# Kernel tuning notes

Hardware: AMD Instinct MI355X
Metric: run time of the kernel (lower is better)

## Reference

```python
import jax, jax.numpy as jnp
import numpy as np

B, S, D, H, L, I, V, T = 8, 512, 768, 12, 6, 3072, 30522, 2
DH = D // H  # 64


def ln2d(x, g, b, eps=1e-5):
    # LayerNorm over the last two dims ([S, D]), affine params shaped [S, D]
    mu = jnp.mean(x, axis=(-2, -1), keepdims=True)
    var = jnp.var(x, axis=(-2, -1), keepdims=True)
    return (x - mu) * jax.lax.rsqrt(var + eps) * g + b


def setup_inputs() -> dict:
    key = jax.random.key(0)
    ks = jax.random.split(key, 16)
    s = 0.02
    inp = {
        "input_ids": jax.random.randint(ks[0], (B, S), 0, V, dtype=jnp.int32),
        "segment_ids": jax.random.randint(ks[1], (B, S), 0, T, dtype=jnp.int32),
        "input_mask": jnp.ones((B, S), dtype=jnp.float32),
        "word_emb": jax.random.normal(ks[2], (V, D), jnp.float32) * s,
        "seg_emb": jax.random.normal(ks[3], (T, D), jnp.float32) * s,
        "pos_emb": jax.random.normal(ks[4], (S, D), jnp.float32) * s,
        "ln0_g": jnp.ones((S, D), jnp.float32),
        "ln0_b": jnp.zeros((S, D), jnp.float32),
        "Wq": jax.random.normal(ks[5], (L, D, D), jnp.float32) * s,
        "Wk": jax.random.normal(ks[6], (L, D, D), jnp.float32) * s,
        "Wv": jax.random.normal(ks[7], (L, D, D), jnp.float32) * s,
        "W1": jax.random.normal(ks[8], (L, D, D), jnp.float32) * s,
        "b1": jnp.zeros((L, D), jnp.float32),
        "Wi": jax.random.normal(ks[9], (L, D, I), jnp.float32) * s,
        "bi": jnp.zeros((L, I), jnp.float32),
        "W2": jax.random.normal(ks[10], (L, I, D), jnp.float32) * s,
        "b2": jnp.zeros((L, D), jnp.float32),
        "lng": jnp.ones((L, S, D), jnp.float32),
        "lnb": jnp.zeros((L, S, D), jnp.float32),
        "Wp": jax.random.normal(ks[11], (D, 2), jnp.float32) * s,
        "bp": jnp.zeros((2,), jnp.float32),
    }
    return inp


def _forward(input_ids, segment_ids, input_mask, word_emb, seg_emb, pos_emb,
             ln0_g, ln0_b, Wq, Wk, Wv, W1, b1, Wi, bi, W2, b2, lng, lnb, Wp, bp):
    # embedding (word + segment + position), then 2-D LayerNorm
    x = word_emb[input_ids] + seg_emb[segment_ids] + pos_emb  # [B,S,D]
    x = ln2d(x, ln0_g, ln0_b)
    # multiplicative attention mask, broadcast over heads and KEY axis
    qmask = input_mask[:, None, :, None]  # [B,1,S,1]
    scale = 1.0 / jnp.sqrt(jnp.asarray(DH, x.dtype))
    for l in range(L):
        prev = x
        q = (x @ Wq[l]).reshape(B, S, H, DH).transpose(0, 2, 1, 3)
        k = (x @ Wk[l]).reshape(B, S, H, DH).transpose(0, 2, 1, 3)
        v = (x @ Wv[l]).reshape(B, S, H, DH).transpose(0, 2, 1, 3)
        scores = jnp.einsum('bhqd,bhkd->bhqk', q, k) * scale
        scores = scores * qmask  # multiplicative mask (as in source)
        probs = jax.nn.softmax(scores, axis=-1)
        attn = jnp.einsum('bhqk,bhkd->bhqd', probs, v)
        attn = attn.transpose(0, 2, 1, 3).reshape(B, S, D)
        h = jax.nn.relu(attn @ W1[l] + b1[l])
        h = jax.nn.relu(h @ Wi[l] + bi[l])
        h = jax.nn.relu(h @ W2[l] + b2[l])
        x = ln2d(h + prev, lng[l], lnb[l])
    logits = x @ Wp + bp  # [B,S,2]
    logits = logits + (1.0 - input_mask)[:, :, None] * (-1e4)
    return logits[:, :, 0], logits[:, :, 1]


def reference(input_ids, segment_ids, input_mask, word_emb, seg_emb, pos_emb,
              ln0_g, ln0_b, Wq, Wk, Wv, W1, b1, Wi, bi, W2, b2, lng, lnb, Wp, bp):
    return _forward(input_ids, segment_ids, input_mask, word_emb, seg_emb, pos_emb,
                    ln0_g, ln0_b, Wq, Wk, Wv, W1, b1, Wi, bi, W2, b2, lng, lnb, Wp, bp)
```

## Files before the change

### kernel.cpp

```cpp
#include <hip/hip_runtime.h>
#include <cstdint>
#include <cstddef>

typedef __bf16 bf16x8 __attribute__((ext_vector_type(8)));
typedef float f32x4 __attribute__((ext_vector_type(4)));
typedef unsigned short u16;

#define NB 8
#define NS 512
#define ND 768
#define NH 12
#define NL 6
#define NI 3072
#define NROWS (NB*NS)
#define SD (NS*ND)
#define MN ((size_t)NROWS*ND)

__device__ __forceinline__ u16 f2bf(float f) {
  union { float f; unsigned u; } v; v.f = f;
  unsigned r = v.u + 0x7fffu + ((v.u >> 16) & 1u);
  return (u16)(r >> 16);
}

#define GLL(gsrc, ldst) \
  __builtin_amdgcn_global_load_lds((__attribute__((address_space(1))) void*)(gsrc), \
                                   (__attribute__((address_space(3))) void*)(ldst), 16, 0, 0)

__global__ __launch_bounds__(256) void wconv_k(
    const float* __restrict__ Wq, const float* __restrict__ Wk, const float* __restrict__ Wv,
    const float* __restrict__ W1, const float* __restrict__ Wi, const float* __restrict__ W2,
    u16* __restrict__ wqkv_t, u16* __restrict__ w1_t, u16* __restrict__ wi_t, u16* __restrict__ w2_t)
{
  int bid = blockIdx.x;
  int l = bid / 1728, r = bid % 1728;
  const float* src; u16* dst; int Csrc, dstLD, tr, tc;
  if (r < 432) {
    int which = r / 144, t = r % 144;
    src = (which == 0 ? Wq : (which == 1 ? Wk : Wv)) + (size_t)l * ND * ND;
    dst = wqkv_t + (size_t)l * 2304 * ND + (size_t)which * ND * ND;
    Csrc = ND; dstLD = ND; tr = t / 12; tc = t % 12;
  } else if (r < 576) {
    int t = r - 432;
    src = W1 + (size_t)l * ND * ND; dst = w1_t + (size_t)l * ND * ND;
    Csrc = ND; dstLD = ND; tr = t / 12; tc = t % 12;
  } else if (r < 1152) {
    int t = r - 576;
    src = Wi + (size_t)l * ND * NI; dst = wi_t + (size_t)l * ND * NI;
    Csrc = NI; dstLD = ND; tr = t / 48; tc = t % 48;
  } else {
    int t = r - 1152;
    src = W2 + (size_t)l * ND * NI; dst = w2_t + (size_t)l * ND * NI;
    Csrc = ND; dstLD = NI; tr = t / 12; tc = t % 12;
  }
  __shared__ u16 tile[64][65];
  int t0 = threadIdx.x;
  int rr = t0 >> 2, c4 = (t0 & 3) * 16;
  const float* sp = src + (size_t)(tr * 64 + rr) * Csrc + tc * 64 + c4;
  #pragma unroll
  for (int q = 0; q < 4; q++) {
    float4 v = reinterpret_cast<const float4*>(sp)[q];
    tile[rr][c4 + q * 4 + 0] = f2bf(v.x);
    tile[rr][c4 + q * 4 + 1] = f2bf(v.y);
    tile[rr][c4 + q * 4 + 2] = f2bf(v.z);
    tile[rr][c4 + q * 4 + 3] = f2bf(v.w);
  }
  __syncthreads();
  int cc = t0 >> 2, r4 = (t0 & 3) * 16;
  u16* dp = dst + (size_t)(tc * 64 + cc) * dstLD + tr * 64 + r4;
  unsigned res[8];
  #pragma unroll
  for (int e = 0; e < 8; e++)
    res[e] = (unsigned)tile[r4 + 2 * e][cc] | ((unsigned)tile[r4 + 2 * e + 1][cc] << 16);
  reinterpret_cast<uint4*>(dp)[0] = make_uint4(res[0], res[1], res[2], res[3]);
  reinterpret_cast<uint4*>(dp + 8)[0] = make_uint4(res[4], res[5], res[6], res[7]);
}

__global__ void embed_k(const int* __restrict__ ids, const int* __restrict__ segs,
    const float* __restrict__ wemb, const float* __restrict__ semb, const float* __restrict__ pemb,
    float* __restrict__ out)
{
  int row = blockIdx.x;
  int s = row & (NS - 1);
  int t = threadIdx.x;
  int id = ids[row], sg = segs[row];
  float4 a = reinterpret_cast<const float4*>(wemb + (size_t)id * ND)[t];
  float4 b = reinterpret_cast<const float4*>(semb + (size_t)sg * ND)[t];
  float4 c = reinterpret_cast<const float4*>(pemb + (size_t)s * ND)[t];
  float4 o;
  o.x = a.x + b.x + c.x; o.y = a.y + b.y + c.y; o.z = a.z + b.z + c.z; o.w = a.w + b.w + c.w;
  reinterpret_cast<float4*>(out + (size_t)row * ND)[t] = o;
}

__global__ __launch_bounds__(256) void ln_part_k(const float* __restrict__ x, float* __restrict__ part)
{
  int b = blockIdx.x >> 6, c = blockIdx.x & 63;
  const float* base = x + (size_t)b * SD + c * 6144;
  int t = threadIdx.x;
  float s = 0.f, sq = 0.f;
  #pragma unroll
  for (int j = 0; j < 6; j++) {
    float4 v = reinterpret_cast<const float4*>(base)[t + j * 256];
    s += v.x + v.y + v.z + v.w;
    sq += v.x * v.x + v.y * v.y + v.z * v.z + v.w * v.w;
  }
  #pragma unroll
  for (int d = 1; d < 64; d <<= 1) { s += __shfl_xor(s, d); sq += __shfl_xor(sq, d); }
  __shared__ float red[8];
  int w = t >> 6, lane = t & 63;
  if (lane == 0) { red[w] = s; red[4 + w] = sq; }
  __syncthreads();
  if (t == 0) {
    part[blockIdx.x * 2 + 0] = red[0] + red[1] + red[2] + red[3];
    part[blockIdx.x * 2 + 1] = red[4] + red[5] + red[6] + red[7];
  }
}

__global__ void ln_final_k(const float* __restrict__ part, float* __restrict__ mv)
{
  int b = blockIdx.x;
  int lane = threadIdx.x;
  float s = part[(b * 64 + lane) * 2 + 0];
  float q = part[(b * 64 + lane) * 2 + 1];
  #pragma unroll
  for (int d = 1; d < 64; d <<= 1) { s += __shfl_xor(s, d); q += __shfl_xor(q, d); }
  if (lane == 0) {
    float inv = 1.f / (float)SD;
    float mu = s * inv;
    float var = q * inv - mu * mu;
    mv[b * 2 + 0] = mu;
    mv[b * 2 + 1] = rsqrtf(var + 1e-5f);
  }
}

__global__ __launch_bounds__(256) void ln_apply_k(const float* __restrict__ x,
    const float* __restrict__ g, const float* __restrict__ bta, const float* __restrict__ mv,
    float* __restrict__ xf, u16* __restrict__ xb)
{
  int idx = blockIdx.x * 256 + threadIdx.x;
  int e = idx * 4;
  int b = e / SD;
  int sd = e - b * SD;
  float mu = mv[b * 2 + 0], rstd = mv[b * 2 + 1];
  float4 v = reinterpret_cast<const float4*>(x)[idx];
  float4 gg = reinterpret_cast<const float4*>(g)[sd >> 2];
  float4 bb = reinterpret_cast<const float4*>(bta)[sd >> 2];
  float y0 = (v.x - mu) * rstd * gg.x + bb.x;
  float y1 = (v.y - mu) * rstd * gg.y + bb.y;
  float y2 = (v.z - mu) * rstd * gg.z + bb.z;
  float y3 = (v.w - mu) * rstd * gg.w + bb.w;
  float4 o; o.x = y0; o.y = y1; o.z = y2; o.w = y3;
  reinterpret_cast<float4*>(xf)[idx] = o;
  reinterpret_cast<ushort4*>(xb)[idx] = make_ushort4(f2bf(y0), f2bf(y1), f2bf(y2), f2bf(y3));
}

__global__ __launch_bounds__(256) void finw2_k(const float* __restrict__ P,
    const float* __restrict__ bias, const float* __restrict__ resid,
    float* __restrict__ ln_in, float* __restrict__ part)
{
  int b = blockIdx.x >> 6, c = blockIdx.x & 63;
  size_t f4base = ((size_t)b * SD + (size_t)c * 6144) >> 2;
  int t = threadIdx.x;
  float s = 0.f, sq = 0.f;
  #pragma unroll
  for (int j = 0; j < 6; j++) {
    size_t fi = f4base + t + j * 256;
    float4 p0 = reinterpret_cast<const float4*>(P)[fi];
    float4 p1 = reinterpret_cast<const float4*>(P)[fi + (MN >> 2)];
    float4 p2 = reinterpret_cast<const float4*>(P)[fi + 2 * (MN >> 2)];
    float4 p3 = reinterpret_cast<const float4*>(P)[fi + 3 * (MN >> 2)];
    float4 rv = reinterpret_cast<const float4*>(resid)[fi];
    int col4 = (((t + j * 256) * 4) % ND) >> 2;
    float4 bv = reinterpret_cast<const float4*>(bias)[col4];
    float y0 = fmaxf(p0.x + p1.x + p2.x + p3.x + bv.x, 0.f) + rv.x;
    float y1 = fmaxf(p0.y + p1.y + p2.y + p3.y + bv.y, 0.f) + rv.y;
    float y2 = fmaxf(p0.z + p1.z + p2.z + p3.z + bv.z, 0.f) + rv.z;
    float y3 = fmaxf(p0.w + p1.w + p2.w + p3.w + bv.w, 0.f) + rv.w;
    float4 o; o.x = y0; o.y = y1; o.z = y2; o.w = y3;
    reinterpret_cast<float4*>(ln_in)[fi] = o;
    s += y0 + y1 + y2 + y3;
    sq += y0 * y0 + y1 * y1 + y2 * y2 + y3 * y3;
  }
  #pragma unroll
  for (int d = 1; d < 64; d <<= 1) { s += __shfl_xor(s, d); sq += __shfl_xor(sq, d); }
  __shared__ float red[8];
  int w = t >> 6, lane = t & 63;
  if (lane == 0) { red[w] = s; red[4 + w] = sq; }
  __syncthreads();
  if (t == 0) {
    part[blockIdx.x * 2 + 0] = red[0] + red[1] + red[2] + red[3];
    part[blockIdx.x * 2 + 1] = red[4] + red[5] + red[6] + red[7];
  }
}

#define BM 128
#define BN 128
#define BK 32

template<int EPI>
__global__ __launch_bounds__(256) void gemm_bt(
    const u16* __restrict__ A, const u16* __restrict__ Bt, void* __restrict__ Cv,
    const float* __restrict__ bias, int M, int N, int K)
{
  __shared__ __align__(16) u16 As[BM * BK];
  __shared__ __align__(16) u16 Bs[BN * BK];
  const int t = threadIdx.x;
  const int lane = t & 63, w = t >> 6;
  const int wr = w >> 1, wc = w & 1;
  const int l15 = lane & 15, lh = lane >> 4;
  const int m0 = blockIdx.y * BM, n0 = blockIdx.x * BN;
  const int Ksub = K / gridDim.z;
  const int Koff = blockIdx.z * Ksub;

  f32x4 acc[4][4];
  const f32x4 z4 = {0.f, 0.f, 0.f, 0.f};
  #pragma unroll
  for (int i = 0; i < 4; i++)
    #pragma unroll
    for (int j = 0; j < 4; j++) acc[i][j] = z4;

  const int ca = t, cb = t + 256;
  const u16* a0p = A + (size_t)(m0 + (ca >> 2)) * K + (ca & 3) * 8;
  const u16* a1p = A + (size_t)(m0 + (cb >> 2)) * K + (cb & 3) * 8;
  const u16* b0p = Bt + (size_t)(n0 + (ca >> 2)) * K + (ca & 3) * 8;
  const u16* b1p = Bt + (size_t)(n0 + (cb >> 2)) * K + (cb & 3) * 8;
  u16* la0 = As + ca * 8; u16* la1 = As + cb * 8;
  u16* lb0 = Bs + ca * 8; u16* lb1 = Bs + cb * 8;

  for (int k0 = Koff; k0 < Koff + Ksub; k0 += BK) {
    __syncthreads();
    GLL(a0p + k0, la0);
    GLL(a1p + k0, la1);
    GLL(b0p + k0, lb0);
    GLL(b1p + k0, lb1);
    __syncthreads();
    bf16x8 af[4], bfr[4];
    #pragma unroll
    for (int i = 0; i < 4; i++)
      af[i] = *reinterpret_cast<const bf16x8*>(&As[(wr * 64 + i * 16 + l15) * BK + lh * 8]);
    #pragma unroll
    for (int j = 0; j < 4; j++)
      bfr[j] = *reinterpret_cast<const bf16x8*>(&Bs[(wc * 64 + j * 16 + l15) * BK + lh * 8]);
    #pragma unroll
    for (int i = 0; i < 4; i++)
      #pragma unroll
      for (int j = 0; j < 4; j++)
        acc[i][j] = __builtin_amdgcn_mfma_f32_16x16x32_bf16(af[i], bfr[j], acc[i][j], 0, 0, 0);
  }

  float* Pout = (float*)Cv + (size_t)blockIdx.z * M * N;
  #pragma unroll
  for (int i = 0; i < 4; i++) {
    int row_b = m0 + wr * 64 + i * 16 + lh * 4;
    #pragma unroll
    for (int j = 0; j < 4; j++) {
      int col = n0 + wc * 64 + j * 16 + l15;
      float bv = (EPI == 1) ? bias[col] : 0.f;
      #pragma unroll
      for (int r = 0; r < 4; r++) {
        size_t off = (size_t)(row_b + r) * N + col;
        float v = acc[i][j][r];
        if (EPI == 1) ((u16*)Cv)[off] = f2bf(fmaxf(v + bv, 0.f));
        else if (EPI == 3) Pout[off] = v;
        else ((u16*)Cv)[off] = f2bf(v);
      }
    }
  }
}

__global__ __launch_bounds__(256) void attn_k(
    const u16* __restrict__ qkv, const float* __restrict__ mask, u16* __restrict__ out)
{
  const int qt = blockIdx.x;
  const int h = blockIdx.y;
  const int b = blockIdx.z;
  __shared__ __align__(16) u16 Qs[128 * 64];
  __shared__ __align__(16) u16 Ks[64 * 72];
  __shared__ __align__(16) u16 Vt[64 * 72];
  __shared__ __align__(16) u16 Pw[4][32 * 72];
  const int t = threadIdx.x, lane = t & 63, w = t >> 6;
  const int l15 = lane & 15, lh = lane >> 4;

  #pragma unroll
  for (int p = 0; p < 4; p++) {
    int c = t + p * 256;
    const u16* src = qkv + (size_t)(b * NS + qt * 128 + (c >> 3)) * 2304 + h * 64 + (c & 7) * 8;
    GLL(src, Qs + c * 8);
  }
  __syncthreads();

  bf16x8 aq[2][2];
  #pragma unroll
  for (int i = 0; i < 2; i++)
    #pragma unroll
    for (int kk = 0; kk < 2; kk++)
      aq[i][kk] = *reinterpret_cast<const bf16x8*>(&Qs[(w * 32 + i * 16 + l15) * 64 + kk * 32 + lh * 8]);

  float qm[2][4];
  #pragma unroll
  for (int i = 0; i < 2; i++)
    #pragma unroll
    for (int r = 0; r < 4; r++)
      qm[i][r] = mask[b * NS + qt * 128 + w * 32 + i * 16 + lh * 4 + r] * 0.125f;

  float mrun[2][4], lrun[2][4];
  f32x4 o[2][4];
  const f32x4 z4 = {0.f, 0.f, 0.f, 0.f};
  #pragma unroll
  for (int i = 0; i < 2; i++)
    #pragma unroll
    for (int r = 0; r < 4; r++) { mrun[i][r] = -3e38f; lrun[i][r] = 0.f; }
  #pragma unroll
  for (int i = 0; i < 2; i++)
    #pragma unroll
    for (int jn = 0; jn < 4; jn++) o[i][jn] = z4;

  for (int kc = 0; kc < 8; kc++) {
    __syncthreads();
    #pragma unroll
    for (int p = 0; p < 2; p++) {
      int k = (t >> 3) + p * 32;
      int dh0 = (t & 7) * 8;
      const u16* ks = qkv + (size_t)(b * NS + kc * 64 + k) * 2304 + ND + h * 64 + dh0;
      uint4 kv4 = *reinterpret_cast<const uint4*>(ks);
      *reinterpret_cast<uint4*>(&Ks[k * 72 + dh0]) = kv4;
    }
    #pragma unroll
    for (int p = 0; p < 2; p++) {
      int k = (t >> 3) + p * 32;
      int dh0 = (t & 7) * 8;
      const u16* vs = qkv + (size_t)(b * NS + kc * 64 + k) * 2304 + 2 * ND + h * 64 + dh0;
      uint4 vv = *reinterpret_cast<const uint4*>(vs);
      Vt[(dh0 + 0) * 72 + k] = (u16)(vv.x & 0xffff);
      Vt[(dh0 + 1) * 72 + k] = (u16)(vv.x >> 16);
      Vt[(dh0 + 2) * 72 + k] = (u16)(vv.y & 0xffff);
      Vt[(dh0 + 3) * 72 + k] = (u16)(vv.y >> 16);
      Vt[(dh0 + 4) * 72 + k] = (u16)(vv.z & 0xffff);
      Vt[(dh0 + 5) * 72 + k] = (u16)(vv.z >> 16);
      Vt[(dh0 + 6) * 72 + k] = (u16)(vv.w & 0xffff);
      Vt[(dh0 + 7) * 72 + k] = (u16)(vv.w >> 16);
    }
    __syncthreads();

    f32x4 s[2][4];
    #pragma unroll
    for (int i = 0; i < 2; i++)
      #pragma unroll
      for (int j = 0; j < 4; j++) s[i][j] = z4;
    #pragma unroll
    for (int kk = 0; kk < 2; kk++) {
      bf16x8 bk[4];
      #pragma unroll
      for (int j = 0; j < 4; j++)
        bk[j] = *reinterpret_cast<const bf16x8*>(&Ks[(j * 16 + l15) * 72 + kk * 32 + lh * 8]);
      #pragma unroll
      for (int i = 0; i < 2; i++)
        #pragma unroll
        for (int j = 0; j < 4; j++)
          s[i][j] = __builtin_amdgcn_mfma_f32_16x16x32_bf16(aq[i][kk], bk[j], s[i][j], 0, 0, 0);
    }

    #pragma unroll
    for (int i = 0; i < 2; i++) {
      #pragma unroll
      for (int r = 0; r < 4; r++) {
        float q4 = qm[i][r];
        float v0 = s[i][0][r] * q4, v1 = s[i][1][r] * q4, v2 = s[i][2][r] * q4, v3 = s[i][3][r] * q4;
        float pm = fmaxf(fmaxf(v0, v1), fmaxf(v2, v3));
        pm = fmaxf(pm, __shfl_xor(pm, 1));
        pm = fmaxf(pm, __shfl_xor(pm, 2));
        pm = fmaxf(pm, __shfl_xor(pm, 4));
        pm = fmaxf(pm, __shfl_xor(pm, 8));
        float mnew = fmaxf(mrun[i][r], pm);
        float corr = __expf(mrun[i][r] - mnew);
        mrun[i][r] = mnew;
        float p0 = __expf(v0 - mnew), p1 = __expf(v1 - mnew);
        float p2 = __expf(v2 - mnew), p3 = __expf(v3 - mnew);
        s[i][0][r] = p0; s[i][1][r] = p1; s[i][2][r] = p2; s[i][3][r] = p3;
        float rs = p0 + p1 + p2 + p3;
        rs += __shfl_xor(rs, 1);
        rs += __shfl_xor(rs, 2);
        rs += __shfl_xor(rs, 4);
        rs += __shfl_xor(rs, 8);
        lrun[i][r] = lrun[i][r] * corr + rs;
        #pragma unroll
        for (int jn = 0; jn < 4; jn++) o[i][jn][r] *= corr;
      }
      #pragma unroll
      for (int j = 0; j < 4; j++)
        #pragma unroll
        for (int r = 0; r < 4; r++)
          Pw[w][(i * 16 + lh * 4 + r) * 72 + j * 16 + l15] = f2bf(s[i][j][r]);
    }

    #pragma unroll
    for (int kk2 = 0; kk2 < 2; kk2++) {
      bf16x8 pa[2], vb[4];
      #pragma unroll
      for (int i = 0; i < 2; i++)
        pa[i] = *reinterpret_cast<const bf16x8*>(&Pw[w][(i * 16 + l15) * 72 + kk2 * 32 + lh * 8]);
      #pragma unroll
      for (int jn = 0; jn < 4; jn++)
        vb[jn] = *reinterpret_cast<const bf16x8*>(&Vt[(jn * 16 + l15) * 72 + kk2 * 32 + lh * 8]);
      #pragma unroll
      for (int i = 0; i < 2; i++)
        #pragma unroll
        for (int jn = 0; jn < 4; jn++)
          o[i][jn] = __builtin_amdgcn_mfma_f32_16x16x32_bf16(pa[i], vb[jn], o[i][jn], 0, 0, 0);
    }
  }

  #pragma unroll
  for (int i = 0; i < 2; i++) {
    #pragma unroll
    for (int r = 0; r < 4; r++) {
      int q = qt * 128 + w * 32 + i * 16 + lh * 4 + r;
      float invl = 1.f / lrun[i][r];
      #pragma unroll
      for (int jn = 0; jn < 4; jn++) {
        int col = h * 64 + jn * 16 + l15;
        out[(size_t)(b * NS + q) * ND + col] = f2bf(o[i][jn][r] * invl);
      }
    }
  }
}

__global__ __launch_bounds__(256) void logits_k(const float* __restrict__ x,
    const float* __restrict__ Wp, const float* __restrict__ bp, const float* __restrict__ mask,
    float* __restrict__ out)
{
  int t = threadIdx.x, lane = t & 63, w = t >> 6;
  int row = blockIdx.x * 4 + w;
  const float* xr = x + (size_t)row * ND;
  float a0 = 0.f, a1 = 0.f;
  for (int i = lane; i < ND; i += 64) {
    float v = xr[i];
    a0 += v * Wp[i * 2 + 0];
    a1 += v * Wp[i * 2 + 1];
  }
  #pragma unroll
  for (int d = 1; d < 64; d <<= 1) { a0 += __shfl_xor(a0, d); a1 += __shfl_xor(a1, d); }
  if (lane == 0) {
    float pen = (1.f - mask[row]) * -10000.f;
    out[row] = a0 + bp[0] + pen;
    out[NROWS + row] = a1 + bp[1] + pen;
  }
}

extern "C" void kernel_launch(void* const* d_in, const int* in_sizes, int n_in,
                              void* d_out, int out_size, void* d_ws, size_t ws_size,
                              hipStream_t stream)
{
  const int* ids = (const int*)d_in[0];
  const int* segs = (const int*)d_in[1];
  const float* mask = (const float*)d_in[2];
  const float* wemb = (const float*)d_in[3];
  const float* semb = (const float*)d_in[4];
  const float* pemb = (const float*)d_in[5];
  const float* ln0g = (const float*)d_in[6];
  const float* ln0b = (const float*)d_in[7];
  const float* Wq = (const float*)d_in[8];
  const float* Wk = (const float*)d_in[9];
  const float* Wv = (const float*)d_in[10];
  const float* W1 = (const float*)d_in[11];
  const float* b1 = (const float*)d_in[12];
  const float* Wi = (const float*)d_in[13];
  const float* bi = (const float*)d_in[14];
  const float* W2 = (const float*)d_in[15];
  const float* b2 = (const float*)d_in[16];
  const float* lng = (const float*)d_in[17];
  const float* lnb = (const float*)d_in[18];
  const float* Wp = (const float*)d_in[19];
  const float* bp = (const float*)d_in[20];

  char* ws = (char*)d_ws;
  size_t o = 0;
  auto alloc = [&](size_t n) { size_t r = o; o += (n + 255) & ~(size_t)255; return r; };
  u16* wqkv_t = (u16*)(ws + alloc((size_t)NL * 2304 * ND * 2));
  u16* w1_t   = (u16*)(ws + alloc((size_t)NL * ND * ND * 2));
  u16* wi_t   = (u16*)(ws + alloc((size_t)NL * ND * NI * 2));
  u16* w2_t   = (u16*)(ws + alloc((size_t)NL * ND * NI * 2));
  float* x_f32 = (float*)(ws + alloc((size_t)NROWS * ND * 4));
  u16* x_bf16  = (u16*)(ws + alloc((size_t)NROWS * ND * 2));
  u16* qkv     = (u16*)(ws + alloc((size_t)NROWS * 2304 * 2));
  u16* attn    = (u16*)(ws + alloc((size_t)NROWS * ND * 2));
  u16* h1      = (u16*)(ws + alloc((size_t)NROWS * ND * 2));
  u16* hi      = (u16*)(ws + alloc((size_t)NROWS * NI * 2));
  float* ln_in = (float*)(ws + alloc((size_t)NROWS * ND * 4));
  float* pbuf  = (float*)(ws + alloc(4 * MN * 4));
  float* part  = (float*)(ws + alloc(512 * 2 * 4));
  float* mv    = (float*)(ws + alloc(64));

  wconv_k<<<NL * 1728, 256, 0, stream>>>(Wq, Wk, Wv, W1, Wi, W2, wqkv_t, w1_t, wi_t, w2_t);
  embed_k<<<NROWS, 192, 0, stream>>>(ids, segs, wemb, semb, pemb, ln_in);
  ln_part_k<<<512, 256, 0, stream>>>(ln_in, part);
  ln_final_k<<<8, 64, 0, stream>>>(part, mv);
  ln_apply_k<<<3072, 256, 0, stream>>>(ln_in, ln0g, ln0b, mv, x_f32, x_bf16);

  for (int l = 0; l < NL; l++) {
    gemm_bt<0><<<dim3(18, 32), 256, 0, stream>>>(x_bf16, wqkv_t + (size_t)l * 2304 * ND, qkv,
                                                 nullptr, NROWS, 2304, ND);
    attn_k<<<dim3(4, NH, NB), 256, 0, stream>>>(qkv, mask, attn);
    gemm_bt<1><<<dim3(6, 32), 256, 0, stream>>>(attn, w1_t + (size_t)l * ND * ND, h1,
                                                b1 + (size_t)l * ND, NROWS, ND, ND);
    gemm_bt<1><<<dim3(24, 32), 256, 0, stream>>>(h1, wi_t + (size_t)l * ND * NI, hi,
                                                 bi + (size_t)l * NI, NROWS, NI, ND);
    gemm_bt<3><<<dim3(6, 32, 4), 256, 0, stream>>>(hi, w2_t + (size_t)l * ND * NI, pbuf,
                                                   nullptr, NROWS, ND, NI);
    finw2_k<<<512, 256, 0, stream>>>(pbuf, b2 + (size_t)l * ND, x_f32, ln_in, part);
    ln_final_k<<<8, 64, 0, stream>>>(part, mv);
    ln_apply_k<<<3072, 256, 0, stream>>>(ln_in, lng + (size_t)l * SD, lnb + (size_t)l * SD, mv, x_f32, x_bf16);
  }

  logits_k<<<1024, 256, 0, stream>>>(x_f32, Wp, bp, mask, (float*)d_out);
}
```

Baseline: 1.194 ms.

## Double-buffer GEMM LDS tiles, split-K the W1 GEMM, and batch weight transposes

The GEMM now double-buffers its A and B LDS tiles, issuing the next K-step's global-to-LDS loads before the current MFMAs and keeping one barrier per iteration. This is meant to overlap load latency with compute. The W1 projection, which had only 192 blocks, now runs as a 4-way split-K into fp32 partials, followed by a new reduce kernel that adds bias, applies ReLU and converts to bf16. This raises GPU occupancy but adds fp32 partial traffic. The weight-conversion kernel now handles four 64x64 tiles per block, cutting the block count by four.

Result: no change. 1.191 ms (-0.3%).

```diff
diff --git a/kernel.cpp b/kernel.cpp
--- a/kernel.cpp
+++ b/kernel.cpp
@@ -26,53 +26,65 @@
   __builtin_amdgcn_global_load_lds((__attribute__((address_space(1))) void*)(gsrc), \
                                    (__attribute__((address_space(3))) void*)(ldst), 16, 0, 0)
 
+#define CHS 4168
+
 __global__ __launch_bounds__(256) void wconv_k(
     const float* __restrict__ Wq, const float* __restrict__ Wk, const float* __restrict__ Wv,
     const float* __restrict__ W1, const float* __restrict__ Wi, const float* __restrict__ W2,
     u16* __restrict__ wqkv_t, u16* __restrict__ w1_t, u16* __restrict__ wi_t, u16* __restrict__ w2_t)
 {
   int bid = blockIdx.x;
-  int l = bid / 1728, r = bid % 1728;
+  int l = bid / 432, r = bid % 432;
   const float* src; u16* dst; int Csrc, dstLD, tr, tc;
-  if (r < 432) {
-    int which = r / 144, t = r % 144;
+  if (r < 108) {
+    int which = r / 36, t2 = r % 36;
     src = (which == 0 ? Wq : (which == 1 ? Wk : Wv)) + (size_t)l * ND * ND;
     dst = wqkv_t + (size_t)l * 2304 * ND + (size_t)which * ND * ND;
-    Csrc = ND; dstLD = ND; tr = t / 12; tc = t % 12;
-  } else if (r < 576) {
-    int t = r - 432;
+    Csrc = ND; dstLD = ND; tr = t2 / 12; tc = t2 % 12;
+  } else if (r < 144) {
+    int t2 = r - 108;
     src = W1 + (size_t)l * ND * ND; dst = w1_t + (size_t)l * ND * ND;
-    Csrc = ND; dstLD = ND; tr = t / 12; tc = t % 12;
-  } else if (r < 1152) {
-    int t = r - 576;
+    Csrc = ND; dstLD = ND; tr = t2 / 12; tc = t2 % 12;
+  } else if (r < 288) {
+    int t2 = r - 144;
     src = Wi + (size_t)l * ND * NI; dst = wi_t + (size_t)l * ND * NI;
-    Csrc = NI; dstLD = ND; tr = t / 48; tc = t % 48;
+    Csrc = NI; dstLD = ND; tr = t2 / 48; tc = t2 % 48;
   } else {
-    int t = r - 1152;
+    int t2 = r - 288;
     src = W2 + (size_t)l * ND * NI; dst = w2_t + (size_t)l * ND * NI;
-    Csrc = ND; dstLD = NI; tr = t / 12; tc = t % 12;
-  }
-  __shared__ u16 tile[64][65];
+    Csrc = ND; dstLD = NI; tr = t2 / 12; tc = t2 % 12;
+  }
+  __shared__ u16 lds[4 * CHS];
   int t0 = threadIdx.x;
-  int rr = t0 >> 2, c4 = (t0 & 3) * 16;
-  const float* sp = src + (size_t)(tr * 64 + rr) * Csrc + tc * 64 + c4;
+  int rr = t0 >> 2, cl = t0 & 3;
   #pragma unroll
   for (int q = 0; q < 4; q++) {
-    float4 v = reinterpret_cast<const float4*>(sp)[q];
-    tile[rr][c4 + q * 4 + 0] = f2bf(v.x);
-    tile[rr][c4 + q * 4 + 1] = f2bf(v.y);
-    tile[rr][c4 + q * 4 + 2] = f2bf(v.z);
-    tile[rr][c4 + q * 4 + 3] = f2bf(v.w);
+    const float* sp = src + (size_t)(tr * 256 + q * 64 + rr) * Csrc + tc * 64 + cl * 4;
+    u16* lp = &lds[q * CHS + rr * 65];
+    #pragma unroll
+    for (int i = 0; i < 4; i++) {
+      float4 v = *reinterpret_cast<const float4*>(sp + i * 16);
+      int c = cl * 4 + i * 16;
+      lp[c + 0] = f2bf(v.x); lp[c + 1] = f2bf(v.y);
+      lp[c + 2] = f2bf(v.z); lp[c + 3] = f2bf(v.w);
+    }
   }
   __syncthreads();
-  int cc = t0 >> 2, r4 = (t0 & 3) * 16;
-  u16* dp = dst + (size_t)(tc * 64 + cc) * dstLD + tr * 64 + r4;
-  unsigned res[8];
-  #pragma unroll
-  for (int e = 0; e < 8; e++)
-    res[e] = (unsigned)tile[r4 + 2 * e][cc] | ((unsigned)tile[r4 + 2 * e + 1][cc] << 16);
-  reinterpret_cast<uint4*>(dp)[0] = make_uint4(res[0], res[1], res[2], res[3]);
-  reinterpret_cast<uint4*>(dp + 8)[0] = make_uint4(res[4], res[5], res[6], res[7]);
+  int cc = t0 >> 2, qq = t0 & 3;
+  u16* dp = dst + (size_t)(tc * 64 + cc) * dstLD + tr * 256;
+  #pragma unroll
+  for (int i = 0; i < 8; i++) {
+    int ch = i >> 1, rbase = (i & 1) * 32 + qq * 8;
+    const u16* lq = &lds[ch * CHS + cc];
+    unsigned res[4];
+    #pragma unroll
+    for (int e = 0; e < 4; e++) {
+      unsigned lo = lq[(rbase + 2 * e) * 65];
+      unsigned hi = lq[(rbase + 2 * e + 1) * 65];
+      res[e] = lo | (hi << 16);
+    }
+    *reinterpret_cast<uint4*>(dp + qq * 8 + i * 32) = make_uint4(res[0], res[1], res[2], res[3]);
+  }
 }
 
 __global__ void embed_k(const int* __restrict__ ids, const int* __restrict__ segs,
@@ -151,6 +163,23 @@
   float4 o; o.x = y0; o.y = y1; o.z = y2; o.w = y3;
   reinterpret_cast<float4*>(xf)[idx] = o;
   reinterpret_cast<ushort4*>(xb)[idx] = make_ushort4(f2bf(y0), f2bf(y1), f2bf(y2), f2bf(y3));
+}
+
+__global__ __launch_bounds__(256) void finw1_k(const float* __restrict__ P,
+    const float* __restrict__ bias, u16* __restrict__ out)
+{
+  size_t idx = (size_t)blockIdx.x * 256 + threadIdx.x;
+  float4 p0 = reinterpret_cast<const float4*>(P)[idx];
+  float4 p1 = reinterpret_cast<const float4*>(P)[idx + (MN >> 2)];
+  float4 p2 = reinterpret_cast<const float4*>(P)[idx + 2 * (MN >> 2)];
+  float4 p3 = reinterpret_cast<const float4*>(P)[idx + 3 * (MN >> 2)];
+  int col4 = (int)((idx * 4) % ND) >> 2;
+  float4 bv = reinterpret_cast<const float4*>(bias)[col4];
+  float y0 = fmaxf(p0.x + p1.x + p2.x + p3.x + bv.x, 0.f);
+  float y1 = fmaxf(p0.y + p1.y + p2.y + p3.y + bv.y, 0.f);
+  float y2 = fmaxf(p0.z + p1.z + p2.z + p3.z + bv.z, 0.f);
+  float y3 = fmaxf(p0.w + p1.w + p2.w + p3.w + bv.w, 0.f);
+  reinterpret_cast<ushort4*>(out)[idx] = make_ushort4(f2bf(y0), f2bf(y1), f2bf(y2), f2bf(y3));
 }
 
 __global__ __launch_bounds__(256) void finw2_k(const float* __restrict__ P,
@@ -201,8 +230,8 @@
     const u16* __restrict__ A, const u16* __restrict__ Bt, void* __restrict__ Cv,
     const float* __restrict__ bias, int M, int N, int K)
 {
-  __shared__ __align__(16) u16 As[BM * BK];
-  __shared__ __align__(16) u16 Bs[BN * BK];
+  __shared__ __align__(16) u16 As[2][BM * BK];
+  __shared__ __align__(16) u16 Bs[2][BN * BK];
   const int t = threadIdx.x;
   const int lane = t & 63, w = t >> 6;
   const int wr = w >> 1, wc = w & 1;
@@ -219,32 +248,37 @@
     for (int j = 0; j < 4; j++) acc[i][j] = z4;
 
   const int ca = t, cb = t + 256;
-  const u16* a0p = A + (size_t)(m0 + (ca >> 2)) * K + (ca & 3) * 8;
-  const u16* a1p = A + (size_t)(m0 + (cb >> 2)) * K + (cb & 3) * 8;
-  const u16* b0p = Bt + (size_t)(n0 + (ca >> 2)) * K + (ca & 3) * 8;
-  const u16* b1p = Bt + (size_t)(n0 + (cb >> 2)) * K + (cb & 3) * 8;
-  u16* la0 = As + ca * 8; u16* la1 = As + cb * 8;
-  u16* lb0 = Bs + ca * 8; u16* lb1 = Bs + cb * 8;
-
-  for (int k0 = Koff; k0 < Koff + Ksub; k0 += BK) {
-    __syncthreads();
-    GLL(a0p + k0, la0);
-    GLL(a1p + k0, la1);
-    GLL(b0p + k0, lb0);
-    GLL(b1p + k0, lb1);
-    __syncthreads();
+  const u16* a0p = A + (size_t)(m0 + (ca >> 2)) * K + (ca & 3) * 8 + Koff;
+  const u16* a1p = A + (size_t)(m0 + (cb >> 2)) * K + (cb & 3) * 8 + Koff;
+  const u16* b0p = Bt + (size_t)(n0 + (ca >> 2)) * K + (ca & 3) * 8 + Koff;
+  const u16* b1p = Bt + (size_t)(n0 + (cb >> 2)) * K + (cb & 3) * 8 + Koff;
+
+  auto stage = [&](int buf, int k0) {
+    GLL(a0p + k0, &As[buf][ca * 8]);
+    GLL(a1p + k0, &As[buf][cb * 8]);
+    GLL(b0p + k0, &Bs[buf][ca * 8]);
+    GLL(b1p + k0, &Bs[buf][cb * 8]);
+  };
+
+  const int nt = Ksub / BK;
+  stage(0, 0);
+  __syncthreads();
+  for (int it = 0; it < nt; ++it) {
+    const int cur = it & 1;
+    if (it + 1 < nt) stage(cur ^ 1, (it + 1) * BK);
     bf16x8 af[4], bfr[4];
     #pragma unroll
     for (int i = 0; i < 4; i++)
-      af[i] = *reinterpret_cast<const bf16x8*>(&As[(wr * 64 + i * 16 + l15) * BK + lh * 8]);
+      af[i] = *reinterpret_cast<const bf16x8*>(&As[cur][(wr * 64 + i * 16 + l15) * BK + lh * 8]);
     #pragma unroll
     for (int j = 0; j < 4; j++)
-      bfr[j] = *reinterpret_cast<const bf16x8*>(&Bs[(wc * 64 + j * 16 + l15) * BK + lh * 8]);
+      bfr[j] = *reinterpret_cast<const bf16x8*>(&Bs[cur][(wc * 64 + j * 16 + l15) * BK + lh * 8]);
     #pragma unroll
     for (int i = 0; i < 4; i++)
       #pragma unroll
       for (int j = 0; j < 4; j++)
         acc[i][j] = __builtin_amdgcn_mfma_f32_16x16x32_bf16(af[i], bfr[j], acc[i][j], 0, 0, 0);
+    __syncthreads();
   }
 
   float* Pout = (float*)Cv + (size_t)blockIdx.z * M * N;
@@ -490,7 +524,7 @@
   float* part  = (float*)(ws + alloc(512 * 2 * 4));
   float* mv    = (float*)(ws + alloc(64));
 
-  wconv_k<<<NL * 1728, 256, 0, stream>>>(Wq, Wk, Wv, W1, Wi, W2, wqkv_t, w1_t, wi_t, w2_t);
+  wconv_k<<<NL * 432, 256, 0, stream>>>(Wq, Wk, Wv, W1, Wi, W2, wqkv_t, w1_t, wi_t, w2_t);
   embed_k<<<NROWS, 192, 0, stream>>>(ids, segs, wemb, semb, pemb, ln_in);
   ln_part_k<<<512, 256, 0, stream>>>(ln_in, part);
   ln_final_k<<<8, 64, 0, stream>>>(part, mv);
@@ -500,8 +534,9 @@
     gemm_bt<0><<<dim3(18, 32), 256, 0, stream>>>(x_bf16, wqkv_t + (size_t)l * 2304 * ND, qkv,
                                                  nullptr, NROWS, 2304, ND);
     attn_k<<<dim3(4, NH, NB), 256, 0, stream>>>(qkv, mask, attn);
-    gemm_bt<1><<<dim3(6, 32), 256, 0, stream>>>(attn, w1_t + (size_t)l * ND * ND, h1,
-                                                b1 + (size_t)l * ND, NROWS, ND, ND);
+    gemm_bt<3><<<dim3(6, 32, 4), 256, 0, stream>>>(attn, w1_t + (size_t)l * ND * ND, pbuf,
+                                                   nullptr, NROWS, ND, ND);
+    finw1_k<<<3072, 256, 0, stream>>>(pbuf, b1 + (size_t)l * ND, h1);
     gemm_bt<1><<<dim3(24, 32), 256, 0, stream>>>(h1, wi_t + (size_t)l * ND * NI, hi,
                                                  bi + (size_t)l * NI, NROWS, NI, ND);
     gemm_bt<3><<<dim3(6, 32, 4), 256, 0, stream>>>(hi, w2_t + (size_t)l * ND * NI, pbuf,
```
